# Kernel tuning notes

Hardware: AMD Instinct MI355X
Metric: run time of the kernel (lower is better)

The kernel has to match this reference:

```python
import jax, jax.numpy as jnp
import numpy as np

BN_EPS = 1e-5


def ball_query(pos, radius, k):
    """PointNet++-style ball query: for each point, the first k point indices
    (in index order) whose distance < radius; shorter lists are padded with the
    first valid index (self is always valid since dist=0). pos: (b,n,3).
    Returns idx: (b,n,k) int32."""
    b, n, _ = pos.shape
    sq = jnp.sum(pos * pos, axis=-1)                       # (b,n)
    d2 = sq[:, :, None] + sq[:, None, :] - 2.0 * jnp.einsum('bnc,bmc->bnm', pos, pos)
    mask = d2 < radius * radius                            # (b,n,n)
    cand = jnp.where(mask, jnp.arange(n, dtype=jnp.int32)[None, None, :], jnp.int32(n))
    # smallest-k indices in ascending order == first-k valid in index order
    neg_top, _ = jax.lax.top_k(-cand, k)                   # (b,n,k)
    idx = -neg_top
    first = idx[..., :1]
    idx = jnp.where(idx == n, first, idx)                  # pad with first neighbor
    return idx


def reference(pos, x, w1, gamma, beta, w2, b2, radius, k):
    pos = jax.lax.stop_gradient(pos)
    idx = ball_query(pos, radius, k)                       # (b,n,k)
    grouped = jax.vmap(lambda p, i: p[i])(pos, idx)        # (b,n,k,3)
    rel = grouped - pos[:, :, None, :]                     # center-subtract
    # 1x1 conv (3->3, no bias)
    h = jnp.einsum('bnkc,dc->bnkd', rel, w1)
    # BatchNorm2d (training-mode batch stats over b,k,n per channel)
    mean = jnp.mean(h, axis=(0, 1, 2))
    var = jnp.mean((h - mean) ** 2, axis=(0, 1, 2))
    h = (h - mean) * jax.lax.rsqrt(var + BN_EPS) * gamma + beta
    h = jax.nn.relu(h)
    # 1x1 conv (3->out_channel) + bias
    pe = jnp.einsum('bnkd,ed->bnke', h, w2) + b2           # (b,n,k,C)
    pe = jnp.max(pe, axis=2)                               # max over k neighbors
    return x + pe


def setup_inputs() -> dict:
    key = jax.random.key(0)
    ks = jax.random.split(key, 5)
    b, n, c, kk = 2, 8192, 64, 32
    pos = jax.random.uniform(ks[0], (b, n, 3), dtype=jnp.float32)
    x = jax.random.normal(ks[1], (b, n, c), dtype=jnp.float32)
    w1 = jax.random.normal(ks[2], (3, 3), dtype=jnp.float32) * 0.5
    gamma = jnp.ones((3,), dtype=jnp.float32)
    beta = jnp.zeros((3,), dtype=jnp.float32)
    w2 = jax.random.normal(ks[3], (c, 3), dtype=jnp.float32) * 0.5
    b2 = jnp.zeros((c,), dtype=jnp.float32)
    radius = jnp.float32(0.1)
    return {"pos": pos, "x": x, "w1": w1, "gamma": gamma, "beta": beta,
            "w2": w2, "b2": b2, "radius": radius, "k": kk}
```

## Files before the change

### kernel.cpp

```cpp
#include <hip/hip_runtime.h>
#include <math.h>

#define NPTS   8192
#define NBATCH 2
#define NQ     (NPTS * NBATCH)
#define KNB    32
#define CFEAT  64
#define BN_EPS 1e-5f

#define MAXC     1000
#define CSTR     1024
#define CAP_HIT  128

#define QBK2  16
#define NBLK2 (NQ / QBK2)

#define QBK3  16
#define NBLK3 (NQ / QBK3)

#define WS_H     0
#define WS_PART  (WS_H + NQ * 3 * KNB)
#define WS_STATS (WS_PART + 6 * NBLK2)
#define WS_HIST  (WS_STATS + 8)
#define WS_CUR   (WS_HIST + 2 * CSTR)
#define WS_CS    (WS_CUR + 2 * CSTR)
#define WS_BIN   (WS_CS + 2 * CSTR)

__device__ __forceinline__ int grid_from_r(double rd) {
    int G = (int)(1.0 / rd);
    if (G < 1) G = 1;
    while (G > 1 && 1.0 / (double)G < rd) --G;
    if (G > 10) G = 10;
    return G;
}

__device__ __forceinline__ int mbcnt64(unsigned long long m) {
    return (int)__builtin_amdgcn_mbcnt_hi((unsigned)(m >> 32),
             __builtin_amdgcn_mbcnt_lo((unsigned)m, 0u));
}

__device__ __forceinline__ int cell_of(float v, float Gf, int G) {
    int c = (int)(v * Gf);
    return c > G - 1 ? G - 1 : c;
}

__global__ __launch_bounds__(256) void kH_hist(
    const float* __restrict__ pos, const float* __restrict__ radius,
    float* __restrict__ ws)
{
    const int p = blockIdx.x * 256 + threadIdx.x;
    const int batch = p >> 13;
    const int pl = p & (NPTS - 1);
    const double rd = (double)radius[0];
    const int G = grid_from_r(rd);
    const float Gf = (float)G;
    const float* pp = pos + (size_t)batch * NPTS * 3 + (size_t)pl * 3;
    float x = pp[0], y = pp[1], z = pp[2];
    int c = (cell_of(z, Gf, G) * G + cell_of(y, Gf, G)) * G + cell_of(x, Gf, G);
    atomicAdd((int*)ws + WS_HIST + batch * CSTR + c, 1);
}

__global__ __launch_bounds__(1024) void kS_scan(
    const float* __restrict__ radius, float* __restrict__ ws)
{
    __shared__ int wtot[16];
    const int tid = threadIdx.x, lane = tid & 63, wave = tid >> 6;
    const double rd = (double)radius[0];
    const int G = grid_from_r(rd);
    const int NC = G * G * G;

    for (int batch = 0; batch < NBATCH; ++batch) {
        const int* hist = (const int*)ws + WS_HIST + batch * CSTR;
        int* cur = (int*)ws + WS_CUR + batch * CSTR;
        int* cs  = (int*)ws + WS_CS  + batch * CSTR;
        int v = (tid < NC) ? hist[tid] : 0;
        int incl = v;
#pragma unroll
        for (int off = 1; off < 64; off <<= 1) {
            int t = __shfl_up(incl, off);
            if (lane >= off) incl += t;
        }
        if (lane == 63) wtot[wave] = incl;
        __syncthreads();
        int base = 0;
#pragma unroll
        for (int w = 0; w < 16; ++w) base += (w < wave) ? wtot[w] : 0;
        int excl = base + incl - v;
        if (tid < NC) { cs[tid] = excl; cur[tid] = excl; }
        if (tid == 0) cs[NC] = NPTS;
        __syncthreads();
    }
}

__global__ __launch_bounds__(256) void kC_scatter(
    const float* __restrict__ pos, const float* __restrict__ radius,
    float* __restrict__ ws)
{
    const int p = blockIdx.x * 256 + threadIdx.x;
    const int batch = p >> 13;
    const int pl = p & (NPTS - 1);
    const double rd = (double)radius[0];
    const int G = grid_from_r(rd);
    const float Gf = (float)G;
    const float* pp = pos + (size_t)batch * NPTS * 3 + (size_t)pl * 3;
    float x = pp[0], y = pp[1], z = pp[2];
    int c = (cell_of(z, Gf, G) * G + cell_of(y, Gf, G)) * G + cell_of(x, Gf, G);
    int slot = atomicAdd((int*)ws + WS_CUR + batch * CSTR + c, 1);
    float4* bin = (float4*)(ws + WS_BIN) + (size_t)batch * NPTS;
    bin[slot] = make_float4(x, y, z, __int_as_float(pl));
}

__global__ __launch_bounds__(256) void k2_query(
    const float* __restrict__ pos, const float* __restrict__ w1,
    const float* __restrict__ radius, float* __restrict__ ws)
{
    __shared__ int   hitl[4][CAP_HIT];
    __shared__ int   seli[4][KNB];
    __shared__ float sred[4][6];

    const int tid = threadIdx.x, lane = tid & 63, wave = tid >> 6;
    const int qbase = blockIdx.x * QBK2;
    const int batch = qbase / NPTS;
    const float* bpos = pos + (size_t)batch * NPTS * 3;
    const double rd  = (double)radius[0];
    const double r2d = rd * rd;
    const int G = grid_from_r(rd);
    const float Gf = (float)G;
    const int* cs = (const int*)ws + WS_CS + batch * CSTR;
    const float4* bin = (const float4*)(ws + WS_BIN) + (size_t)batch * NPTS;

    float w1r[9];
#pragma unroll
    for (int i = 0; i < 9; ++i) w1r[i] = w1[i];

    float ls0 = 0.f, ls1 = 0.f, ls2 = 0.f;
    float lq0 = 0.f, lq1 = 0.f, lq2 = 0.f;

#pragma unroll 1
    for (int qq = 0; qq < 4; ++qq) {
        const int qg = qbase + wave * 4 + qq;
        const int ql = qg - batch * NPTS;
        const float qx = bpos[ql * 3], qy = bpos[ql * 3 + 1], qz = bpos[ql * 3 + 2];
        const double qxd = (double)qx, qyd = (double)qy, qzd = (double)qz;
        const double qsd = fma(qzd, qzd, fma(qyd, qyd, qxd * qxd));
        const int cx = cell_of(qx, Gf, G);
        const int cy = cell_of(qy, Gf, G);
        const int cz = cell_of(qz, Gf, G);
        const int cx0 = max(cx - 1, 0), cx1 = min(cx + 1, G - 1);

        int rs0[9], rpref[10];
        int tot = 0;
#pragma unroll
        for (int r = 0; r < 9; ++r) {
            const int ny = cy + (r % 3) - 1;
            const int nz = cz + (r / 3) - 1;
            int s0 = 0, len = 0;
            if (ny >= 0 && ny < G && nz >= 0 && nz < G) {
                const int cb = (nz * G + ny) * G;
                s0  = cs[cb + cx0];
                len = cs[cb + cx1 + 1] - s0;
            }
            rs0[r] = s0; rpref[r] = tot; tot += len;
        }
        rpref[9] = tot;

        int hc = 0;
        for (int b0 = 0; b0 < tot; b0 += 64) {
            const int flat = b0 + lane;
            const bool act = flat < tot;
            int ss = flat + (rs0[0] - rpref[0]);
#pragma unroll
            for (int i = 1; i < 9; ++i)
                ss += (flat >= rpref[i]) ? ((rs0[i] - rpref[i]) -
                                            (rs0[i - 1] - rpref[i - 1])) : 0;
            float4 P = bin[act ? ss : 0];
            double xj = (double)P.x, yj = (double)P.y, zj = (double)P.z;
            double sqj = fma(zj, zj, fma(yj, yj, xj * xj));
            double dot = fma(zj, qzd, fma(yj, qyd, xj * qxd));
            double dd  = (qsd + sqj) - 2.0 * dot;
            bool in = act && (dd < r2d);
            unsigned long long bal = __ballot(in);
            if (in) {
                int p2 = hc + mbcnt64(bal);
                if (p2 < CAP_HIT) hitl[wave][p2] = __float_as_int(P.w);
            }
            hc += (int)__popcll(bal);
        }
        if (hc > CAP_HIT) hc = CAP_HIT;

        if (hc <= KNB) {
            int v = (lane < hc) ? hitl[wave][lane] : 0x7FFFFFFF;
            int mn = v;
#pragma unroll
            for (int off = 32; off; off >>= 1) mn = min(mn, __shfl_xor(mn, off));
            if (lane < KNB) seli[wave][lane] = (lane < hc) ? v : mn;
        } else {
            int a = (lane < hc) ? hitl[wave][lane] : 0x7FFFFFFF;
            int b = (64 + lane < hc) ? hitl[wave][64 + lane] : 0x7FFFFFFF;
            int lo = 0, hi = NPTS - 1;
            while (lo < hi) {
                int mid = (lo + hi) >> 1;
                int c1 = (int)__popcll(__ballot(a <= mid)) +
                         (int)__popcll(__ballot(b <= mid));
                if (c1 >= KNB) hi = mid; else lo = mid + 1;
            }
            const int t = lo;
            unsigned long long ba = __ballot(a <= t);
            unsigned long long bb = __ballot(b <= t);
            int na = (int)__popcll(ba);
            if (a <= t) seli[wave][mbcnt64(ba)] = a;
            if (b <= t) seli[wave][na + mbcnt64(bb)] = b;
        }

        if (lane < KNB) {
            int j = seli[wave][lane];
            const float* pj = bpos + (size_t)j * 3;
            float rx = __fsub_rn(pj[0], qx);
            float ry = __fsub_rn(pj[1], qy);
            float rz = __fsub_rn(pj[2], qz);
            float h0 = fmaf(rz, w1r[2], fmaf(ry, w1r[1], __fmul_rn(rx, w1r[0])));
            float h1 = fmaf(rz, w1r[5], fmaf(ry, w1r[4], __fmul_rn(rx, w1r[3])));
            float h2 = fmaf(rz, w1r[8], fmaf(ry, w1r[7], __fmul_rn(rx, w1r[6])));
            float* hout = ws + WS_H + (size_t)qg * 3 * KNB;
            hout[0 * KNB + lane] = h0;
            hout[1 * KNB + lane] = h1;
            hout[2 * KNB + lane] = h2;
            ls0 += h0; ls1 += h1; ls2 += h2;
            lq0 += h0 * h0; lq1 += h1 * h1; lq2 += h2 * h2;
        }
    }

#pragma unroll
    for (int m = 1; m < 64; m <<= 1) {
        ls0 += __shfl_xor(ls0, m); ls1 += __shfl_xor(ls1, m); ls2 += __shfl_xor(ls2, m);
        lq0 += __shfl_xor(lq0, m); lq1 += __shfl_xor(lq1, m); lq2 += __shfl_xor(lq2, m);
    }
    if (lane == 0) {
        sred[wave][0] = ls0; sred[wave][1] = ls1; sred[wave][2] = ls2;
        sred[wave][3] = lq0; sred[wave][4] = lq1; sred[wave][5] = lq2;
    }
    __syncthreads();
    if (tid < 6) {
        float s = sred[0][tid] + sred[1][tid] + sred[2][tid] + sred[3][tid];
        ws[WS_PART + tid * NBLK2 + blockIdx.x] = s;
    }
}

__global__ __launch_bounds__(1024) void k2b_stats(float* __restrict__ ws)
{
    __shared__ float wred[16][6];
    const int tid = threadIdx.x, lane = tid & 63, wave = tid >> 6;

#pragma unroll
    for (int c = 0; c < 6; ++c) {
        float s = ws[WS_PART + c * NBLK2 + tid];
#pragma unroll
        for (int m = 1; m < 64; m <<= 1) s += __shfl_xor(s, m);
        if (lane == 0) wred[wave][c] = s;
    }
    __syncthreads();
    if (tid < 3) {
        const double N = (double)((long long)NQ * KNB);
        double s = 0.0, sq = 0.0;
#pragma unroll
        for (int w = 0; w < 16; ++w) { s += wred[w][tid]; sq += wred[w][3 + tid]; }
        double mean = s / N;
        double var  = sq / N - mean * mean;
        ws[WS_STATS + tid]     = (float)mean;
        ws[WS_STATS + 3 + tid] = (float)(1.0 / sqrt(var + (double)BN_EPS));
    }
}

__global__ __launch_bounds__(256) void k3_mlp(
    const float* __restrict__ ws, const float* __restrict__ gamma,
    const float* __restrict__ beta, const float* __restrict__ w2,
    const float* __restrict__ b2, const float* __restrict__ x,
    float* __restrict__ out)
{
    __shared__ float gl[QBK3 * 96];

    const int tid = threadIdx.x;
    const float m0 = ws[WS_STATS + 0], m1 = ws[WS_STATS + 1], m2 = ws[WS_STATS + 2];
    const float i0 = ws[WS_STATS + 3], i1 = ws[WS_STATS + 4], i2 = ws[WS_STATS + 5];
    const float g0 = gamma[0], g1 = gamma[1], g2 = gamma[2];
    const float b0 = beta[0],  b1 = beta[1],  b2c = beta[2];

    const int qbase = blockIdx.x * QBK3;
    const float* hin = ws + WS_H + (size_t)qbase * 96;

#pragma unroll
    for (int r = 0; r < 6; ++r) {
        const int idx = r * 256 + tid;
        const int c = (idx % 96) >> 5;
        float h = hin[idx];
        float mm = c == 0 ? m0 : (c == 1 ? m1 : m2);
        float ii = c == 0 ? i0 : (c == 1 ? i1 : i2);
        float gg = c == 0 ? g0 : (c == 1 ? g1 : g2);
        float bb = c == 0 ? b0 : (c == 1 ? b1 : b2c);
        float n = __fadd_rn(__fmul_rn(__fmul_rn(__fsub_rn(h, mm), ii), gg), bb);
        gl[idx] = fmaxf(n, 0.0f);
    }
    __syncthreads();

    const int ch = tid & 63;
    const int qh = tid >> 6;
    const float w20 = w2[ch * 3 + 0];
    const float w21 = w2[ch * 3 + 1];
    const float w22 = w2[ch * 3 + 2];
    const float bias = b2[ch];

#pragma unroll
    for (int r = 0; r < 4; ++r) {
        const int q = r * 4 + qh;
        const float* gq = &gl[q * 96];
        float m = -INFINITY;
#pragma unroll 4
        for (int kk = 0; kk < KNB; ++kk) {
            float ga = gq[kk], gb = gq[32 + kk], gc = gq[64 + kk];
            float pe = __fadd_rn(fmaf(gc, w22, fmaf(gb, w21, __fmul_rn(ga, w20))), bias);
            m = fmaxf(m, pe);
        }
        const size_t o = (size_t)(qbase + q) * CFEAT + ch;
        out[o] = __fadd_rn(x[o], m);
    }
}

extern "C" void kernel_launch(void* const* d_in, const int* in_sizes, int n_in,
                              void* d_out, int out_size, void* d_ws, size_t ws_size,
                              hipStream_t stream) {
    (void)in_sizes; (void)n_in; (void)out_size; (void)ws_size;
    const float* pos    = (const float*)d_in[0];
    const float* x      = (const float*)d_in[1];
    const float* w1     = (const float*)d_in[2];
    const float* gamma  = (const float*)d_in[3];
    const float* beta   = (const float*)d_in[4];
    const float* w2     = (const float*)d_in[5];
    const float* b2     = (const float*)d_in[6];
    const float* radius = (const float*)d_in[7];
    float* out = (float*)d_out;
    float* ws  = (float*)d_ws;

    hipMemsetAsync(ws + WS_HIST, 0, 2 * CSTR * sizeof(int), stream);
    hipLaunchKernelGGL(kH_hist,    dim3(NQ / 256), dim3(256),  0, stream, pos, radius, ws);
    hipLaunchKernelGGL(kS_scan,    dim3(1),        dim3(1024), 0, stream, radius, ws);
    hipLaunchKernelGGL(kC_scatter, dim3(NQ / 256), dim3(256),  0, stream, pos, radius, ws);
    hipLaunchKernelGGL(k2_query,   dim3(NBLK2),    dim3(256),  0, stream, pos, w1, radius, ws);
    hipLaunchKernelGGL(k2b_stats,  dim3(1),        dim3(1024), 0, stream, ws);
    hipLaunchKernelGGL(k3_mlp,     dim3(NBLK3),    dim3(256),  0, stream,
                       ws, gamma, beta, w2, b2, x, out);
}
```

Before: 66.03 us.

## Fuse binning into one per-batch kernel and fold stats into query tail

Replaces the memset, histogram, scan and scatter launches with a single kernel, one 1024-thread block per batch, that does the histogram, scan and scatter in shared memory. The separate BN-stats kernel is removed: the last k2_query block to finish, detected with a global atomic counter and threadfence, reduces the per-block partial sums. This cuts four launches and their inter-kernel gaps. The cost is that binning now runs on only two workgroups, serialising the point loops, and every query block pays an extra fence and atomic.

```diff
diff --git a/kernel.cpp b/kernel.cpp
--- a/kernel.cpp
+++ b/kernel.cpp
@@ -21,9 +21,8 @@
 #define WS_H     0
 #define WS_PART  (WS_H + NQ * 3 * KNB)
 #define WS_STATS (WS_PART + 6 * NBLK2)
-#define WS_HIST  (WS_STATS + 8)
-#define WS_CUR   (WS_HIST + 2 * CSTR)
-#define WS_CS    (WS_CUR + 2 * CSTR)
+#define WS_CNT   (WS_STATS + 6)
+#define WS_CS    (WS_STATS + 8)
 #define WS_BIN   (WS_CS + 2 * CSTR)
 
 __device__ __forceinline__ int grid_from_r(double rd) {
@@ -44,70 +43,62 @@
     return c > G - 1 ? G - 1 : c;
 }
 
-__global__ __launch_bounds__(256) void kH_hist(
+__global__ __launch_bounds__(1024) void kBin(
     const float* __restrict__ pos, const float* __restrict__ radius,
     float* __restrict__ ws)
 {
-    const int p = blockIdx.x * 256 + threadIdx.x;
-    const int batch = p >> 13;
-    const int pl = p & (NPTS - 1);
+    __shared__ int hist[MAXC];
+    __shared__ int cur[MAXC];
+    __shared__ int wtot[16];
+
+    const int tid = threadIdx.x, lane = tid & 63, wave = tid >> 6;
+    const int batch = blockIdx.x;
+    if (batch == 0 && tid == 0) ((int*)ws)[WS_CNT] = 0;
+
+    const float* bpos = pos + (size_t)batch * NPTS * 3;
     const double rd = (double)radius[0];
     const int G = grid_from_r(rd);
     const float Gf = (float)G;
-    const float* pp = pos + (size_t)batch * NPTS * 3 + (size_t)pl * 3;
-    float x = pp[0], y = pp[1], z = pp[2];
-    int c = (cell_of(z, Gf, G) * G + cell_of(y, Gf, G)) * G + cell_of(x, Gf, G);
-    atomicAdd((int*)ws + WS_HIST + batch * CSTR + c, 1);
-}
-
-__global__ __launch_bounds__(1024) void kS_scan(
-    const float* __restrict__ radius, float* __restrict__ ws)
-{
-    __shared__ int wtot[16];
-    const int tid = threadIdx.x, lane = tid & 63, wave = tid >> 6;
-    const double rd = (double)radius[0];
-    const int G = grid_from_r(rd);
     const int NC = G * G * G;
 
-    for (int batch = 0; batch < NBATCH; ++batch) {
-        const int* hist = (const int*)ws + WS_HIST + batch * CSTR;
-        int* cur = (int*)ws + WS_CUR + batch * CSTR;
-        int* cs  = (int*)ws + WS_CS  + batch * CSTR;
-        int v = (tid < NC) ? hist[tid] : 0;
-        int incl = v;
-#pragma unroll
-        for (int off = 1; off < 64; off <<= 1) {
-            int t = __shfl_up(incl, off);
-            if (lane >= off) incl += t;
-        }
-        if (lane == 63) wtot[wave] = incl;
-        __syncthreads();
-        int base = 0;
-#pragma unroll
-        for (int w = 0; w < 16; ++w) base += (w < wave) ? wtot[w] : 0;
-        int excl = base + incl - v;
-        if (tid < NC) { cs[tid] = excl; cur[tid] = excl; }
-        if (tid == 0) cs[NC] = NPTS;
-        __syncthreads();
-    }
-}
-
-__global__ __launch_bounds__(256) void kC_scatter(
-    const float* __restrict__ pos, const float* __restrict__ radius,
-    float* __restrict__ ws)
-{
-    const int p = blockIdx.x * 256 + threadIdx.x;
-    const int batch = p >> 13;
-    const int pl = p & (NPTS - 1);
-    const double rd = (double)radius[0];
-    const int G = grid_from_r(rd);
-    const float Gf = (float)G;
-    const float* pp = pos + (size_t)batch * NPTS * 3 + (size_t)pl * 3;
-    float x = pp[0], y = pp[1], z = pp[2];
-    int c = (cell_of(z, Gf, G) * G + cell_of(y, Gf, G)) * G + cell_of(x, Gf, G);
-    int slot = atomicAdd((int*)ws + WS_CUR + batch * CSTR + c, 1);
+    for (int c = tid; c < NC; c += 1024) hist[c] = 0;
+    __syncthreads();
+
+    for (int p = tid; p < NPTS; p += 1024) {
+        const float* pp = bpos + (size_t)p * 3;
+        int c = (cell_of(pp[2], Gf, G) * G + cell_of(pp[1], Gf, G)) * G
+                + cell_of(pp[0], Gf, G);
+        atomicAdd(&hist[c], 1);
+    }
+    __syncthreads();
+
+    int v = (tid < NC) ? hist[tid] : 0;
+    int incl = v;
+#pragma unroll
+    for (int off = 1; off < 64; off <<= 1) {
+        int t = __shfl_up(incl, off);
+        if (lane >= off) incl += t;
+    }
+    if (lane == 63) wtot[wave] = incl;
+    __syncthreads();
+    int base = 0;
+#pragma unroll
+    for (int w = 0; w < 16; ++w) base += (w < wave) ? wtot[w] : 0;
+    const int excl = base + incl - v;
+    int* cs = (int*)ws + WS_CS + batch * CSTR;
+    if (tid < NC) { cs[tid] = excl; cur[tid] = excl; }
+    if (tid == 0) cs[NC] = NPTS;
+    __syncthreads();
+
     float4* bin = (float4*)(ws + WS_BIN) + (size_t)batch * NPTS;
-    bin[slot] = make_float4(x, y, z, __int_as_float(pl));
+    for (int p = tid; p < NPTS; p += 1024) {
+        const float* pp = bpos + (size_t)p * 3;
+        float x = pp[0], y = pp[1], z = pp[2];
+        int c = (cell_of(z, Gf, G) * G + cell_of(y, Gf, G)) * G
+                + cell_of(x, Gf, G);
+        int slot = atomicAdd(&cur[c], 1);
+        bin[slot] = make_float4(x, y, z, __int_as_float(p));
+    }
 }
 
 __global__ __launch_bounds__(256) void k2_query(
@@ -117,6 +108,8 @@
     __shared__ int   hitl[4][CAP_HIT];
     __shared__ int   seli[4][KNB];
     __shared__ float sred[4][6];
+    __shared__ float wred[4][6];
+    __shared__ int   slast;
 
     const int tid = threadIdx.x, lane = tid & 63, wave = tid >> 6;
     const int qbase = blockIdx.x * QBK2;
@@ -244,16 +237,29 @@
         float s = sred[0][tid] + sred[1][tid] + sred[2][tid] + sred[3][tid];
         ws[WS_PART + tid * NBLK2 + blockIdx.x] = s;
     }
-}
-
-__global__ __launch_bounds__(1024) void k2b_stats(float* __restrict__ ws)
-{
-    __shared__ float wred[16][6];
-    const int tid = threadIdx.x, lane = tid & 63, wave = tid >> 6;
-
+
+    __threadfence();
+    __syncthreads();
+    if (tid == 0) {
+        int prev = atomicAdd((int*)ws + WS_CNT, 1);
+        slast = (prev == NBLK2 - 1);
+    }
+    __syncthreads();
+    if (!slast) return;
+
+    float acc[6];
 #pragma unroll
     for (int c = 0; c < 6; ++c) {
-        float s = ws[WS_PART + c * NBLK2 + tid];
+        float s = 0.f;
+        for (int i = tid; i < NBLK2; i += 256) {
+            s += __hip_atomic_load(&ws[WS_PART + c * NBLK2 + i],
+                                   __ATOMIC_RELAXED, __HIP_MEMORY_SCOPE_AGENT);
+        }
+        acc[c] = s;
+    }
+#pragma unroll
+    for (int c = 0; c < 6; ++c) {
+        float s = acc[c];
 #pragma unroll
         for (int m = 1; m < 64; m <<= 1) s += __shfl_xor(s, m);
         if (lane == 0) wred[wave][c] = s;
@@ -263,7 +269,7 @@
         const double N = (double)((long long)NQ * KNB);
         double s = 0.0, sq = 0.0;
 #pragma unroll
-        for (int w = 0; w < 16; ++w) { s += wred[w][tid]; sq += wred[w][3 + tid]; }
+        for (int w = 0; w < 4; ++w) { s += wred[w][tid]; sq += wred[w][3 + tid]; }
         double mean = s / N;
         double var  = sq / N - mean * mean;
         ws[WS_STATS + tid]     = (float)mean;
@@ -340,12 +346,8 @@
     float* out = (float*)d_out;
     float* ws  = (float*)d_ws;
 
-    hipMemsetAsync(ws + WS_HIST, 0, 2 * CSTR * sizeof(int), stream);
-    hipLaunchKernelGGL(kH_hist,    dim3(NQ / 256), dim3(256),  0, stream, pos, radius, ws);
-    hipLaunchKernelGGL(kS_scan,    dim3(1),        dim3(1024), 0, stream, radius, ws);
-    hipLaunchKernelGGL(kC_scatter, dim3(NQ / 256), dim3(256),  0, stream, pos, radius, ws);
-    hipLaunchKernelGGL(k2_query,   dim3(NBLK2),    dim3(256),  0, stream, pos, w1, radius, ws);
-    hipLaunchKernelGGL(k2b_stats,  dim3(1),        dim3(1024), 0, stream, ws);
-    hipLaunchKernelGGL(k3_mlp,     dim3(NBLK3),    dim3(256),  0, stream,
+    hipLaunchKernelGGL(kBin,     dim3(NBATCH), dim3(1024), 0, stream, pos, radius, ws);
+    hipLaunchKernelGGL(k2_query, dim3(NBLK2),  dim3(256),  0, stream, pos, w1, radius, ws);
+    hipLaunchKernelGGL(k3_mlp,   dim3(NBLK3),  dim3(256),  0, stream,
                        ws, gamma, beta, w2, b2, x, out);
 }
```

Result: slower. 134.8 us (+104.1%).
